# Optimization experiments

Measured on AMD Instinct MI355X. Metric: run time of the kernel, lower is better.

The kernel has to match this reference:

```python
import jax, jax.numpy as jnp
import numpy as np

LN_EPS = 1e-5


def _layernorm(h, gamma, beta):
    mu = jnp.mean(h, axis=-1, keepdims=True)
    var = jnp.var(h, axis=-1, keepdims=True)
    return (h - mu) * jax.lax.rsqrt(var + LN_EPS) * gamma + beta


def _simple_attention(q, k, v):
    # DIFFormer 'simple' kernel, num_heads=1: global-Frobenius-normalized q,k,
    # linear attention numerator + uniform component, denominator + N.
    n = q.shape[0]
    qs = q / jnp.linalg.norm(q)            # [N, M]
    ks = k / jnp.linalg.norm(k)            # [N, M]
    kvs = jnp.einsum('lm,ld->md', ks, v)   # [M, D]
    num = jnp.einsum('nm,md->nd', qs, kvs) + jnp.sum(v, axis=0)  # [N, D]
    den = jnp.einsum('nm,m->n', qs, jnp.sum(ks, axis=0)) + jnp.asarray(n, q.dtype)
    return num / den[:, None]


def reference(x, edge_index, W1, b1, Wq, bq, Wk, bk, gamma, beta, alpha, Wr, br, wgt):
    n = x.shape[0]
    row, col = edge_index[0], edge_index[1]
    # symmetric GCN normalization (degree of destination index, as in DIFFormer)
    deg = jax.ops.segment_sum(jnp.ones_like(col, dtype=x.dtype), col, num_segments=n)
    inv_sqrt = jnp.where(deg > 0, 1.0 / jnp.sqrt(deg), 0.0)
    w_edge = inv_sqrt[col] * inv_sqrt[row]  # [E]

    def gcn_conv(v):
        # out[i] = sum_{e: col[e]==i} w[e] * v[row[e]]
        return jax.ops.segment_sum(w_edge[:, None] * v[row], col, num_segments=n)

    def conv(h):
        q = h @ Wq + bq
        k = h @ Wk + bk
        v = h                              # use_weight=False -> value = source input
        return _simple_attention(q, k, v) + gcn_conv(v)

    R = jax.nn.relu(x @ W1 + b1)           # [N, H]
    Ts = [R]
    for _ in range(3):                      # three calls of the SAME shared conv
        Rn = conv(R)
        R = alpha * Rn + (1.0 - alpha) * R  # residual blend
        R = _layernorm(R, gamma, beta)      # shared LayerNorm
        Ts.append(R)

    # multi-head linear readout + learned weighted sum (dropout = identity in eval)
    res = jnp.stack([Ts[i] @ Wr[i] + br[i] for i in range(4)], axis=0)  # [4, N]
    out = jnp.einsum('i,in->n', wgt, res)[:, None]                       # [N, 1]
    return out


def setup_inputs():
    key = jax.random.key(0)
    ks = jax.random.split(key, 8)
    N, E, F_IN, H = 100000, 3200000, 58, 256
    x = jax.random.normal(ks[0], (N, F_IN), dtype=jnp.float32)
    edge_index = jax.random.randint(ks[1], (2, E), 0, N, dtype=jnp.int32)
    s_in = 1.0 / np.sqrt(F_IN)
    s_h = 1.0 / np.sqrt(H)
    return {
        'x': x,
        'edge_index': edge_index,
        'W1': jax.random.normal(ks[2], (F_IN, H), dtype=jnp.float32) * s_in,
        'b1': jnp.zeros((H,), jnp.float32),
        'Wq': jax.random.normal(ks[3], (H, H), dtype=jnp.float32) * s_h,
        'bq': jnp.zeros((H,), jnp.float32),
        'Wk': jax.random.normal(ks[4], (H, H), dtype=jnp.float32) * s_h,
        'bk': jnp.zeros((H,), jnp.float32),
        'gamma': jnp.ones((H,), jnp.float32),
        'beta': jnp.zeros((H,), jnp.float32),
        'alpha': jnp.float32(0.5),
        'Wr': jax.random.normal(ks[5], (4, H), dtype=jnp.float32) * s_h,
        'br': jnp.zeros((4,), jnp.float32),
        'wgt': jnp.array([0.5, 0.5, 0.5, 0.5], jnp.float32),
    }
```

## Files before the change

kernel.cpp:

```cpp
#include <hip/hip_runtime.h>

#define H 256
#define FIN 58
#define LN_EPS 1e-5f
#define ROWS_PB 384
#define EPB 8192
#define SBW 11

typedef __bf16 bf16x8 __attribute__((ext_vector_type(8)));
typedef float f32x16 __attribute__((ext_vector_type(16)));
typedef float f32x2 __attribute__((ext_vector_type(2)));

union FragU {
  ushort u[8];
  bf16x8 v;
};


__device__ __forceinline__ float wave_sum(float v) {
#pragma unroll
  for (int off = 1; off < 64; off <<= 1) v += __shfl_xor(v, off, 64);
  return v;
}

__device__ __forceinline__ float half_sum(float v) {
#pragma unroll
  for (int off = 1; off < 32; off <<= 1) v += __shfl_xor(v, off, 64);
  return v;
}

__device__ __forceinline__ float block_sum(float v, volatile float* red) {
  const int tid = threadIdx.x;
  v = wave_sum(v);
  __syncthreads();
  if ((tid & 63) == 0) red[tid >> 6] = v;
  __syncthreads();
  return red[0] + red[1] + red[2] + red[3];
}

__device__ __forceinline__ ushort f2bf(float f) {
  unsigned u = __float_as_uint(f);
  unsigned r = (u + 0x7FFFu + ((u >> 16) & 1u)) >> 16;
  return (ushort)r;
}

__device__ __forceinline__ float bf2f(ushort u) {
  return __uint_as_float((unsigned)u << 16);
}

#if __has_builtin(__builtin_amdgcn_cvt_pk_fp8_f32) && __has_builtin(__builtin_amdgcn_cvt_pk_f32_fp8)
__device__ __forceinline__ unsigned pack_fp8x4(float a, float b, float c, float d) {
  int v = 0;
  v = __builtin_amdgcn_cvt_pk_fp8_f32(a, b, v, false);
  v = __builtin_amdgcn_cvt_pk_fp8_f32(c, d, v, true);
  return (unsigned)v;
}
__device__ __forceinline__ void unpack_fp8x2_acc(f32x2& lo, f32x2& hi, unsigned v) {
  lo += __builtin_amdgcn_cvt_pk_f32_fp8((int)v, false);
  hi += __builtin_amdgcn_cvt_pk_f32_fp8((int)v, true);
}
#else
__device__ __forceinline__ unsigned char f2e4m3_1(float f) {
  unsigned u = __float_as_uint(f);
  unsigned s = (u >> 31) << 7;
  float a = fabsf(f);
  if (a >= 448.0f) return (unsigned char)(s | 0x7E);
  if (a < 0.0009765625f) return (unsigned char)s;
  int e;
  float m = frexpf(a, &e);
  int E = e - 1 + 7;
  if (E >= 1) {
    int mm = (int)rintf((m * 2.0f - 1.0f) * 8.0f);
    if (mm == 8) { mm = 0; E++; }
    return (unsigned char)(s | (E << 3) | mm);
  }
  int mm = (int)rintf(a * 512.0f);
  if (mm > 7) return (unsigned char)(s | (1 << 3));
  return (unsigned char)(s | mm);
}
__device__ __forceinline__ unsigned pack_fp8x4(float a, float b, float c, float d) {
  return (unsigned)f2e4m3_1(a) | ((unsigned)f2e4m3_1(b) << 8) |
         ((unsigned)f2e4m3_1(c) << 16) | ((unsigned)f2e4m3_1(d) << 24);
}
__device__ __forceinline__ float e4m3f_1(unsigned v) {
  int s = (v >> 7) & 1, E = (v >> 3) & 15, m = v & 7;
  float mag = E ? ldexpf(1.0f + m * 0.125f, E - 7) : ldexpf((float)m, -9);
  return s ? -mag : mag;
}
__device__ __forceinline__ void unpack_fp8x2_acc(f32x2& lo, f32x2& hi, unsigned v) {
  lo[0] += e4m3f_1(v & 255);
  lo[1] += e4m3f_1((v >> 8) & 255);
  hi[0] += e4m3f_1((v >> 16) & 255);
  hi[1] += e4m3f_1(v >> 24);
}
#endif


__global__ __launch_bounds__(512) void k_b1(const int* __restrict__ row,
                                            const int* __restrict__ col,
                                            unsigned* __restrict__ breg,
                                            int* __restrict__ gcnt,
                                            int cap2, int E, int nsb) {
  __shared__ unsigned stage[EPB];
  __shared__ int lh[65], lbase[65], lcur[64], gclaim[64];
  const int tid = threadIdx.x;
  const int e0 = blockIdx.x * EPB;
  const int cnt = min(EPB, E - e0);
  if (tid < 64) lh[tid] = 0;
  __syncthreads();
  for (int i = tid; i < cnt; i += 512) atomicAdd(&lh[col[e0 + i] >> SBW], 1);
  __syncthreads();
  if (tid == 0) {
    int acc = 0;
    for (int b = 0; b < nsb; b++) { lbase[b] = acc; acc += lh[b]; }
    lbase[nsb] = acc;
  }
  __syncthreads();
  if (tid < nsb) {
    gclaim[tid] = atomicAdd(&gcnt[tid], lh[tid]);
    lcur[tid] = lbase[tid];
  }
  __syncthreads();
  for (int i = tid; i < cnt; i += 512) {
    int c = col[e0 + i];
    int b = c >> SBW;
    int s = atomicAdd(&lcur[b], 1);
    stage[s] = ((unsigned)row[e0 + i] << SBW) | (unsigned)(c & ((1 << SBW) - 1));
  }
  __syncthreads();
  for (int i = tid; i < cnt; i += 512) {
    int lo = 0, hi = nsb;
    while (hi - lo > 1) {
      int mid = (lo + hi) >> 1;
      if (lbase[mid] <= i) lo = mid; else hi = mid;
    }
    int off = gclaim[lo] + (i - lbase[lo]);
    if (off < cap2) breg[(size_t)lo * cap2 + off] = stage[i];
  }
}

__global__ __launch_bounds__(512) void k_degB2(const unsigned* __restrict__ breg,
                                               const int* __restrict__ gcnt, int cap2,
                                               int* __restrict__ deg, int N) {
  __shared__ int lcnt[1 << SBW];
  const int b = blockIdx.x, tid = threadIdx.x, base = b << SBW;
  for (int i = tid; i < (1 << SBW); i += 512) lcnt[i] = 0;
  __syncthreads();
  const int cnt = min(gcnt[b], cap2);
  const unsigned* p = breg + (size_t)b * cap2;
  for (int i = tid; i < cnt; i += 512) atomicAdd(&lcnt[p[i] & ((1 << SBW) - 1)], 1);
  __syncthreads();
  for (int i = tid; i < (1 << SBW); i += 512) {
    int d = base + i;
    if (d < N) deg[d] = lcnt[i];
  }
}

__global__ __launch_bounds__(512) void k_b2(const unsigned* __restrict__ breg,
                                            const int* __restrict__ gcnt, int cap2,
                                            const int* __restrict__ offs16,
                                            int* __restrict__ eb, int N) {
  __shared__ int loffs[1 << SBW];
  __shared__ int lcur[1 << SBW];
  const int b = blockIdx.x, tid = threadIdx.x, base = b << SBW;
  for (int i = tid; i < (1 << SBW); i += 512) {
    int d = base + i;
    loffs[i] = (d < N) ? offs16[d] : 0;
    lcur[i] = 0;
  }
  __syncthreads();
  const int cnt = min(gcnt[b], cap2);
  const unsigned* p = breg + (size_t)b * cap2;
  for (int i = tid; i < cnt; i += 512) {
    unsigned rc = p[i];
    int lc = rc & ((1 << SBW) - 1);
    int slot = atomicAdd(&lcur[lc], 1);
    eb[loffs[lc] + slot] = (int)(rc >> SBW);
  }
  __syncthreads();
  for (int i = tid; i < (1 << SBW); i += 512) {
    int d = base + i;
    if (d < N) {
      int c = lcur[i];
      int pad = (c + 15) & ~15;
      int o = loffs[i];
      for (int j = c; j < pad; j++) eb[o + j] = N;
    }
  }
}

__global__ void k_invsqrt(const int* __restrict__ deg, float* __restrict__ invs, int N) {
  int i = blockIdx.x * 256 + threadIdx.x;
  if (i < N) {
    int d = deg[i];
    invs[i] = (d > 0) ? (1.0f / sqrtf((float)d)) : 0.0f;
  }
}

__global__ __launch_bounds__(1024) void k_scan1(const int* __restrict__ deg,
                                                int* __restrict__ offs16,
                                                int* __restrict__ bsum, int N) {
  __shared__ int buf[1024];
  const int tid = threadIdx.x;
  const int gid = blockIdx.x * 1024 + tid;
  int v = (gid < N) ? ((deg[gid] + 15) & ~15) : 0;
  buf[tid] = v;
  __syncthreads();
  for (int off = 1; off < 1024; off <<= 1) {
    int x = (tid >= off) ? buf[tid - off] : 0;
    __syncthreads();
    buf[tid] += x;
    __syncthreads();
  }
  if (gid < N) offs16[gid] = buf[tid] - v;
  if (tid == 1023) bsum[blockIdx.x] = buf[1023];
}

__global__ __launch_bounds__(1024) void k_scan2(int* __restrict__ bsum, int nb) {
  __shared__ int buf[1024];
  const int tid = threadIdx.x;
  int v = (tid < nb) ? bsum[tid] : 0;
  buf[tid] = v;
  __syncthreads();
  for (int off = 1; off < 1024; off <<= 1) {
    int x = (tid >= off) ? buf[tid - off] : 0;
    __syncthreads();
    buf[tid] += x;
    __syncthreads();
  }
  if (tid < nb) bsum[tid] = buf[tid] - v;
}

__global__ void k_scan3(int* __restrict__ offs16, const int* __restrict__ bsum, int N) {
  int i = blockIdx.x * 256 + threadIdx.x;
  if (i < N) offs16[i] += bsum[i >> 10];
}

__global__ void k_prep(const float* __restrict__ Wq, const float* __restrict__ Wk,
                       const float* __restrict__ bq, const float* __restrict__ bk,
                       float* __restrict__ P, float* __restrict__ Q, float* __restrict__ K2,
                       float* __restrict__ pb, float* __restrict__ qb,
                       float* __restrict__ wb, float* __restrict__ kb,
                       float* __restrict__ sconst) {
  __shared__ float red[4];
  const int b = blockIdx.x, tid = threadIdx.x;
  if (b < 768) {
    const int f = b & 255, which = b >> 8;
    const float* A = (which == 2) ? Wk : Wq;
    const float* Bm = (which == 1) ? Wq : Wk;
    float acc = 0.0f;
    for (int m = 0; m < H; m++) acc = fmaf(A[f * H + m], Bm[tid * H + m], acc);
    float* D = (which == 0) ? P : ((which == 1) ? Q : K2);
    D[f * H + tid] = acc;
  } else {
    float a1 = 0, a2 = 0, a3 = 0, a4 = 0;
    for (int m = 0; m < H; m++) {
      float wqv = Wq[tid * H + m], wkv = Wk[tid * H + m];
      a1 = fmaf(wqv, bk[m], a1);
      a2 = fmaf(wqv, bq[m], a2);
      a3 = fmaf(wkv, bq[m], a3);
      a4 = fmaf(wkv, bk[m], a4);
    }
    pb[tid] = a1; qb[tid] = a2; wb[tid] = a3; kb[tid] = a4;
    float c0 = block_sum(bq[tid] * bk[tid], red);
    float c1 = block_sum(bq[tid] * bq[tid], red);
    float c2 = block_sum(bk[tid] * bk[tid], red);
    if (tid == 0) { sconst[0] = c0; sconst[1] = c1; sconst[2] = c2; }
  }
}

__global__ void k_fc1(const float* __restrict__ x, const float* __restrict__ W1,
                      const float* __restrict__ b1, const float* __restrict__ Wr,
                      const float* __restrict__ br, const float* __restrict__ wgt,
                      ushort* __restrict__ R0, float* __restrict__ out, int N) {
  __shared__ __align__(16) float lx[16 * FIN];
  __shared__ float red2[4][16];
  const int tid = threadIdx.x;
  const int n0 = blockIdx.x * 16;
  for (int idx = tid; idx < 16 * FIN / 4; idx += 256)
    ((float4*)lx)[idx] = ((const float4*)(x + (size_t)n0 * FIN))[idx];
  __syncthreads();
  float acc[16];
  const float bias = b1[tid];
#pragma unroll
  for (int r = 0; r < 16; r++) acc[r] = bias;
  for (int f = 0; f < FIN; f++) {
    float wv = W1[f * H + tid];
#pragma unroll
    for (int r = 0; r < 16; r++) acc[r] = fmaf(lx[r * FIN + f], wv, acc[r]);
  }
  const float wr0 = Wr[tid];
#pragma unroll
  for (int r = 0; r < 16; r++) {
    acc[r] = fmaxf(acc[r], 0.0f);
    int n = n0 + r;
    if (n < N) R0[(size_t)n * H + tid] = f2bf(acc[r]);
  }
#pragma unroll
  for (int r = 0; r < 16; r++) {
    float s = wave_sum(acc[r] * wr0);
    if ((tid & 63) == 0) red2[tid >> 6][r] = s;
  }
  __syncthreads();
  if (tid < 16) {
    int n = n0 + tid;
    if (n < N)
      out[n] = wgt[0] * (red2[0][tid] + red2[1][tid] + red2[2][tid] + red2[3][tid] + br[0]);
  }
}

__global__ __launch_bounds__(512, 2) void k_Gm(const ushort* __restrict__ Rb,
                                               const float* __restrict__ invs,
                                               ushort* __restrict__ Gslab,
                                               unsigned* __restrict__ Rf8,
                                               float* __restrict__ vsum, int N) {
  __shared__ ushort sb[2][32 * 256];
  const int tid = threadIdx.x;
  const int lane = tid & 63;
  const int wid = tid >> 6;
  const int wrow = (wid & 1) * 128;
  const int wcol = (wid >> 1) * 64;
  const int l31 = lane & 31;
  const int lhi = lane >> 5;

  const int rowbase = blockIdx.x * ROWS_PB;
  const int nrows = min(ROWS_PB, N - rowbase);
  const int nch = (nrows + 31) >> 5;

  const int sk = tid >> 4;
  const int c0 = (tid & 15) * 16;

  f32x16 acc[4][2];
#pragma unroll
  for (int s = 0; s < 4; s++)
#pragma unroll
    for (int t = 0; t < 2; t++)
#pragma unroll
      for (int e = 0; e < 16; e++) acc[s][t][e] = 0.0f;

  float csum[16];
#pragma unroll
  for (int i = 0; i < 16; i++) csum[i] = 0.0f;

  int4 ld[2];

  auto load_chunk = [&](int ch) {
    int g = rowbase + ch * 32 + sk;
    const int4* src = (const int4*)(Rb + (size_t)g * H + c0);
    ld[0] = (g < N) ? src[0] : make_int4(0, 0, 0, 0);
    ld[1] = (g < N) ? src[1] : make_int4(0, 0, 0, 0);
  };

  auto write_chunk = [&](int ch, int buf) {
    int g = rowbase + ch * 32 + sk;
    const int swz = (sk & 3) << 4;
    const float sc = (g < N) ? invs[g] : 0.0f;
    unsigned w8[4];
#pragma unroll
    for (int i = 0; i < 2; i++) {
      *(int4*)&sb[buf][sk * 256 + ((c0 + 8 * i) ^ swz)] = ld[i];
      const ushort* pu = (const ushort*)&ld[i];
#pragma unroll
      for (int j = 0; j < 8; j++) csum[8 * i + j] += bf2f(pu[j]);
      w8[2 * i] = pack_fp8x4(bf2f(pu[0]) * sc, bf2f(pu[1]) * sc,
                             bf2f(pu[2]) * sc, bf2f(pu[3]) * sc);
      w8[2 * i + 1] = pack_fp8x4(bf2f(pu[4]) * sc, bf2f(pu[5]) * sc,
                                 bf2f(pu[6]) * sc, bf2f(pu[7]) * sc);
    }
    if (g < N)
      *(uint4*)&Rf8[(size_t)g * 64 + (c0 >> 2)] = make_uint4(w8[0], w8[1], w8[2], w8[3]);
  };

  auto compute = [&](int buf) {
#pragma unroll
    for (int ks = 0; ks < 2; ks++) {
      const int kb = ks * 16 + lhi * 8;
      FragU fr[6];
#pragma unroll
      for (int s = 0; s < 6; s++) {
        const int cbase = (s < 4) ? (wrow + 32 * s + l31) : (wcol + 32 * (s - 4) + l31);
#pragma unroll
        for (int j = 0; j < 8; j++)
          fr[s].u[j] = sb[buf][(kb + j) * 256 + (cbase ^ ((j & 3) << 4))];
      }
#pragma unroll
      for (int s = 0; s < 4; s++)
#pragma unroll
        for (int t = 0; t < 2; t++)
          acc[s][t] = __builtin_amdgcn_mfma_f32_32x32x16_bf16(fr[s].v, fr[4 + t].v,
                                                              acc[s][t], 0, 0, 0);
    }
  };

  if (nch > 0) {
    load_chunk(0);
    write_chunk(0, 0);
    __syncthreads();
    int cur = 0;
    for (int c = 0; c < nch; c++) {
      if (c + 1 < nch) load_chunk(c + 1);
      compute(cur);
      if (c + 1 < nch) write_chunk(c + 1, cur ^ 1);
      __syncthreads();
      cur ^= 1;
    }
  }

  ushort* Gs = Gslab + (size_t)blockIdx.x * 65536;
#pragma unroll
  for (int s = 0; s < 4; s++)
#pragma unroll
    for (int t = 0; t < 2; t++) {
      const int n0c = wcol + 32 * t + l31;
#pragma unroll
      for (int r = 0; r < 16; r++) {
        const int row = wrow + 32 * s + (r & 3) + 8 * (r >> 2) + 4 * lhi;
        Gs[row * 256 + n0c] = f2bf(acc[s][t][r]);
      }
    }

  float* fl = (float*)sb;
#pragma unroll
  for (int j = 0; j < 16; j++) fl[sk * 256 + c0 + j] = csum[j];
  __syncthreads();
  if (tid < 256) {
    float s = 0.0f;
    for (int r = 0; r < 32; r++) s += fl[r * 256 + tid];
    atomicAdd(&vsum[tid], s);
  }
}

__global__ void k_Gr(const ushort* __restrict__ Gslab, float* __restrict__ G, int nslab) {
  const int i = blockIdx.x * 256 + threadIdx.x;
  float s0 = 0, s1 = 0, s2 = 0, s3 = 0;
  int b = 0;
  for (; b + 3 < nslab; b += 4) {
    s0 += bf2f(Gslab[(size_t)b * 65536 + i]);
    s1 += bf2f(Gslab[(size_t)(b + 1) * 65536 + i]);
    s2 += bf2f(Gslab[(size_t)(b + 2) * 65536 + i]);
    s3 += bf2f(Gslab[(size_t)(b + 3) * 65536 + i]);
  }
  float s = s0 + s1 + s2 + s3;
  for (; b < nslab; b++) s += bf2f(Gslab[(size_t)b * 65536 + i]);
  G[i] = s;
}

__global__ void k_small(const float* __restrict__ G, const float* __restrict__ vsum,
                        const float* __restrict__ P, const float* __restrict__ pb,
                        const float* __restrict__ wb, const float* __restrict__ sconst,
                        const float* __restrict__ Q, const float* __restrict__ K2,
                        ushort* __restrict__ Mt, float* __restrict__ cvec,
                        float* __restrict__ dvec, float* __restrict__ scal, int N) {
  __shared__ float red[4];
  const int b = blockIdx.x, tid = threadIdx.x;
  if (b < 256) {
    float acc = 0.0f;
    for (int m = 0; m < H; m++) acc = fmaf(P[b * H + m], G[m * H + tid], acc);
    Mt[(size_t)tid * H + b] = f2bf(acc + pb[b] * vsum[tid]);
  } else if (b == 256) {
    float acc = 0.0f;
    for (int f = 0; f < H; f++) acc = fmaf(wb[f], G[f * H + tid], acc);
    cvec[tid] = acc + sconst[0] * vsum[tid];
  } else if (b == 257) {
    float acc = 0.0f;
    for (int m = 0; m < H; m++) acc = fmaf(P[tid * H + m], vsum[m], acc);
    dvec[tid] = acc + (float)N * pb[tid];
  } else if (b < 274) {
    int base = (b - 258) * 4096 + tid;
    float a = 0.0f;
    for (int j = 0; j < 16; j++) a = fmaf(G[base + j * 256], Q[base + j * 256], a);
    a = block_sum(a, red);
    if (tid == 0) atomicAdd(&scal[0], a);
  } else {
    int base = (b - 274) * 4096 + tid;
    float a = 0.0f;
    for (int j = 0; j < 16; j++) a = fmaf(G[base + j * 256], K2[base + j * 256], a);
    a = block_sum(a, red);
    if (tid == 0) atomicAdd(&scal[1], a);
  }
}

__global__ void k_final(const float* __restrict__ vsum, const float* __restrict__ qb,
                        const float* __restrict__ kb, const float* __restrict__ wb,
                        const float* __restrict__ sconst, float* __restrict__ scal, int N) {
  __shared__ float red[4];
  const int tid = threadIdx.x;
  float s1 = block_sum(qb[tid] * vsum[tid], red);
  float s2 = block_sum(kb[tid] * vsum[tid], red);
  float s3 = block_sum(wb[tid] * vsum[tid], red);
  if (tid == 0) {
    float sq = scal[0] + 2.0f * s1 + (float)N * sconst[1];
    float sk = scal[1] + 2.0f * s2 + (float)N * sconst[2];
    scal[2] = 1.0f / (sqrtf(sq) * sqrtf(sk));
    scal[3] = s3 + (float)N * sconst[0];
  }
}

__global__ __launch_bounds__(512) void k_N(const ushort* __restrict__ Rb,
                                           const ushort* __restrict__ Mt,
                                           ushort* __restrict__ numb, int N) {
  const int tid = threadIdx.x;
  const int lane = tid & 63;
  const int wid = tid >> 6;
  const int l31 = lane & 31;
  const int lhi = lane >> 5;
  const int wrow = (wid & 3) * 32;
  const int wcol = (wid >> 2) * 128;
  const int rowbase = blockIdx.x * 128;

  f32x16 acc[4];
#pragma unroll
  for (int t = 0; t < 4; t++)
#pragma unroll
    for (int e = 0; e < 16; e++) acc[t][e] = 0.0f;

  const ushort* aptr = Rb + (size_t)(rowbase + wrow + l31) * H;

  for (int kc = 0; kc < 16; kc++) {
    const int kb = kc * 16 + lhi * 8;
    FragU fa;
    *(int4*)fa.u = *(const int4*)(aptr + kb);
    FragU fb0, fb1, fb2, fb3;
    *(int4*)fb0.u = *(const int4*)(Mt + (size_t)(wcol + 0 + l31) * H + kb);
    *(int4*)fb1.u = *(const int4*)(Mt + (size_t)(wcol + 32 + l31) * H + kb);
    *(int4*)fb2.u = *(const int4*)(Mt + (size_t)(wcol + 64 + l31) * H + kb);
    *(int4*)fb3.u = *(const int4*)(Mt + (size_t)(wcol + 96 + l31) * H + kb);
    acc[0] = __builtin_amdgcn_mfma_f32_32x32x16_bf16(fa.v, fb0.v, acc[0], 0, 0, 0);
    acc[1] = __builtin_amdgcn_mfma_f32_32x32x16_bf16(fa.v, fb1.v, acc[1], 0, 0, 0);
    acc[2] = __builtin_amdgcn_mfma_f32_32x32x16_bf16(fa.v, fb2.v, acc[2], 0, 0, 0);
    acc[3] = __builtin_amdgcn_mfma_f32_32x32x16_bf16(fa.v, fb3.v, acc[3], 0, 0, 0);
  }

#pragma unroll
  for (int t = 0; t < 4; t++) {
    const int col = wcol + 32 * t + l31;
#pragma unroll
    for (int r = 0; r < 16; r++) {
      const int row = rowbase + wrow + (r & 3) + 8 * (r >> 2) + 4 * lhi;
      if (row < N) numb[(size_t)row * H + col] = f2bf(acc[t][r]);
    }
  }
}

__global__ __launch_bounds__(256) void k_C(
    const ushort* __restrict__ Rb, ushort* __restrict__ Rnext,
    const ushort* __restrict__ numb, const unsigned* __restrict__ Rf8,
    const int* __restrict__ eb, const float* __restrict__ invs,
    const float* __restrict__ cvec, const float* __restrict__ dvec,
    const float* __restrict__ vsum, const float* __restrict__ scal,
    const int* __restrict__ offs16, const int* __restrict__ deg,
    const float* __restrict__ alphap, const float* __restrict__ gamma,
    const float* __restrict__ beta, const float* __restrict__ Wr,
    const float* __restrict__ br, const float* __restrict__ wgt,
    float* __restrict__ out, int N, int layer, int last) {
  const int tid = threadIdx.x, lane = tid & 63, wv = tid >> 6;
  const int half = lane >> 5, hl = lane & 31;
  const int d0 = hl * 8;
  const int n0 = blockIdx.x * 32 + wv * 8;

  const float invn = scal[2], denc = scal[3];
  const float al = alphap[0], om = 1.0f - al;
  const float4 dvA = *(const float4*)&dvec[d0];
  const float4 dvB = *(const float4*)&dvec[d0 + 4];
  const float4 cvA = *(const float4*)&cvec[d0];
  const float4 cvB = *(const float4*)&cvec[d0 + 4];
  const float4 vsA = *(const float4*)&vsum[d0];
  const float4 vsB = *(const float4*)&vsum[d0 + 4];
  const float4 gmA = *(const float4*)&gamma[d0];
  const float4 gmB = *(const float4*)&gamma[d0 + 4];
  const float4 btA = *(const float4*)&beta[d0];
  const float4 btB = *(const float4*)&beta[d0 + 4];
  const float4 wrA = *(const float4*)&Wr[layer * H + d0];
  const float4 wrB = *(const float4*)&Wr[layer * H + d0 + 4];
  const float wl = wgt[layer], bl = br[layer];

  for (int r = 0; r < 4; r++) {
    const int n = n0 + r * 2 + half;
    const bool valid = n < N;
    const int ns = valid ? n : 0;

    const int4 rv = *(const int4*)&Rb[(size_t)ns * H + d0];
    const int4 nv = *(const int4*)&numb[(size_t)ns * H + d0];
    const ushort* rp = (const ushort*)&rv;
    const ushort* np = (const ushort*)&nv;
    float old[8], num[8];
#pragma unroll
    for (int j = 0; j < 8; j++) { old[j] = bf2f(rp[j]); num[j] = bf2f(np[j]); }

    float p = old[0] * dvA.x + old[1] * dvA.y + old[2] * dvA.z + old[3] * dvA.w +
              old[4] * dvB.x + old[5] * dvB.y + old[6] * dvB.z + old[7] * dvB.w;
    p = half_sum(p);
    const float rden = 1.0f / ((p + denc) * invn + (float)N);

    f32x2 a01 = {0.f, 0.f}, a23 = {0.f, 0.f}, a45 = {0.f, 0.f}, a67 = {0.f, 0.f};
    const int st = offs16[ns];
    const int nbch = valid ? ((deg[ns] + 15) >> 4) : 0;
    const int4* pe = (const int4*)(eb + st);
    const int woff = hl * 2;
    for (int b = 0; b < nbch; b++, pe += 4) {
      int4 q0 = pe[0], q1 = pe[1], q2 = pe[2], q3 = pe[3];
      const int srcs[16] = {q0.x, q0.y, q0.z, q0.w, q1.x, q1.y, q1.z, q1.w,
                            q2.x, q2.y, q2.z, q2.w, q3.x, q3.y, q3.z, q3.w};
      uint2 g[16];
#pragma unroll
      for (int i = 0; i < 16; i++)
        g[i] = *(const uint2*)&Rf8[((size_t)srcs[i] << 6) + woff];
#pragma unroll
      for (int i = 0; i < 16; i++) {
        unpack_fp8x2_acc(a01, a23, g[i].x);
        unpack_fp8x2_acc(a45, a67, g[i].y);
      }
    }
    const float sn = invs[ns];
    float ag[8] = {a01[0] * sn, a01[1] * sn, a23[0] * sn, a23[1] * sn,
                   a45[0] * sn, a45[1] * sn, a67[0] * sn, a67[1] * sn};

    const float cva[8] = {cvA.x, cvA.y, cvA.z, cvA.w, cvB.x, cvB.y, cvB.z, cvB.w};
    const float vsa[8] = {vsA.x, vsA.y, vsA.z, vsA.w, vsB.x, vsB.y, vsB.z, vsB.w};
    float hv[8];
#pragma unroll
    for (int j = 0; j < 8; j++)
      hv[j] = al * (((num[j] + cva[j]) * invn + vsa[j]) * rden + ag[j]) + om * old[j];

    float s = 0.0f, s2 = 0.0f;
#pragma unroll
    for (int j = 0; j < 8; j++) { s += hv[j]; s2 += hv[j] * hv[j]; }
    s = half_sum(s);
    s2 = half_sum(s2);
    const float mu = s * (1.0f / H);
    const float var = s2 * (1.0f / H) - mu * mu;
    const float rs = rsqrtf(var + LN_EPS);

    const float gma[8] = {gmA.x, gmA.y, gmA.z, gmA.w, gmB.x, gmB.y, gmB.z, gmB.w};
    const float bta[8] = {btA.x, btA.y, btA.z, btA.w, btB.x, btB.y, btB.z, btB.w};
    const float wra[8] = {wrA.x, wrA.y, wrA.z, wrA.w, wrB.x, wrB.y, wrB.z, wrB.w};
    float y[8], rp2 = 0.0f;
    ushort yo[8];
#pragma unroll
    for (int j = 0; j < 8; j++) {
      y[j] = (hv[j] - mu) * rs * gma[j] + bta[j];
      yo[j] = f2bf(y[j]);
      rp2 += y[j] * wra[j];
    }
    if (!last && valid) *(int4*)&Rnext[(size_t)n * H + d0] = *(int4*)yo;
    rp2 = half_sum(rp2);
    if (hl == 0 && valid) out[n] += wl * (rp2 + bl);
  }
}


extern "C" void kernel_launch(void* const* d_in, const int* in_sizes, int n_in,
                              void* d_out, int out_size, void* d_ws, size_t ws_size,
                              hipStream_t stream) {
  const float* x = (const float*)d_in[0];
  const int* ei = (const int*)d_in[1];
  const float* W1 = (const float*)d_in[2];
  const float* b1 = (const float*)d_in[3];
  const float* Wq = (const float*)d_in[4];
  const float* bq = (const float*)d_in[5];
  const float* Wk = (const float*)d_in[6];
  const float* bk = (const float*)d_in[7];
  const float* gamma = (const float*)d_in[8];
  const float* beta = (const float*)d_in[9];
  const float* alphap = (const float*)d_in[10];
  const float* Wr = (const float*)d_in[11];
  const float* br = (const float*)d_in[12];
  const float* wgt = (const float*)d_in[13];
  float* out = (float*)d_out;

  const int N = in_sizes[0] / FIN;
  const int E = in_sizes[1] / 2;
  const int* row = ei;
  const int* col = ei + E;

  char* w = (char*)d_ws;
  auto alloc = [&](size_t bytes) -> char* {
    char* p = w;
    w += (bytes + 255) & ~(size_t)255;
    return p;
  };
  const size_t RB = (size_t)(N + 128) * H * sizeof(ushort);
  ushort* Rb0 = (ushort*)alloc(RB);
  ushort* Rb1 = (ushort*)alloc(RB);
  ushort* numb = (ushort*)alloc(RB);
  unsigned* Rf8 = (unsigned*)alloc((size_t)(N + 1) * 64 * sizeof(unsigned));
  ushort* Mt = (ushort*)alloc(H * H * sizeof(ushort));
  float* G = (float*)alloc(H * H * sizeof(float));
  float* vsum = (float*)alloc(1024);
  float* scal = (float*)alloc(256);
  float* cvec = (float*)alloc(1024);
  float* dvec = (float*)alloc(1024);
  float* P = (float*)alloc(H * H * sizeof(float));
  float* Q = (float*)alloc(H * H * sizeof(float));
  float* K2 = (float*)alloc(H * H * sizeof(float));
  float* pb = (float*)alloc(1024);
  float* qb = (float*)alloc(1024);
  float* wb = (float*)alloc(1024);
  float* kb = (float*)alloc(1024);
  float* sconst = (float*)alloc(256);
  int* deg = (int*)alloc((size_t)N * 4);
  float* invs = (float*)alloc((size_t)N * 4);
  int* offs16 = (int*)alloc((size_t)(N + 1) * 4);
  int* bsum = (int*)alloc(1024 * 4);
  int* gcnt = (int*)alloc(64 * 4);
  size_t EPAD = (size_t)E + 16 * (size_t)N;
  EPAD = (EPAD + 3) & ~(size_t)3;
  int* eb = (int*)alloc(EPAD * sizeof(int));

  const int NSB = (N + (1 << SBW) - 1) >> SBW;
  int cap2 = (E / (NSB > 0 ? NSB : 1)) * 2 + 4096;
  cap2 = (cap2 + 3) & ~3;
  unsigned* breg = (unsigned*)Rb1;
  ushort* Gslab = (ushort*)numb;

  hipMemsetAsync(gcnt, 0, 64 * 4, stream);
  hipMemsetAsync(Rf8 + (size_t)N * 64, 0, 64 * sizeof(unsigned), stream);

  const int gN = (N + 255) / 256;
  const int nblk = (N + 1023) / 1024;
  const int nbB1 = (E + EPB - 1) / EPB;
  k_b1<<<nbB1, 512, 0, stream>>>(row, col, breg, gcnt, cap2, E, NSB);
  k_degB2<<<NSB, 512, 0, stream>>>(breg, gcnt, cap2, deg, N);
  k_invsqrt<<<gN, 256, 0, stream>>>(deg, invs, N);
  k_scan1<<<nblk, 1024, 0, stream>>>(deg, offs16, bsum, N);
  k_scan2<<<1, 1024, 0, stream>>>(bsum, nblk);
  k_scan3<<<gN, 256, 0, stream>>>(offs16, bsum, N);
  k_b2<<<NSB, 512, 0, stream>>>(breg, gcnt, cap2, offs16, eb, N);
  k_prep<<<769, 256, 0, stream>>>(Wq, Wk, bq, bk, P, Q, K2, pb, qb, wb, kb, sconst);
  const int gRows16 = (N + 15) / 16;
  k_fc1<<<gRows16, 256, 0, stream>>>(x, W1, b1, Wr, br, wgt, Rb0, out, N);

  const int nbG = (N + ROWS_PB - 1) / ROWS_PB;
  const int nbN = (N + 127) / 128;
  const int gRows32 = (N + 31) / 32;
  ushort* Rc = Rb0;
  ushort* Rn = Rb1;
  for (int it = 1; it <= 3; ++it) {
    hipMemsetAsync(vsum, 0, 1024 + 256, stream);
    k_Gm<<<nbG, 512, 0, stream>>>(Rc, invs, Gslab, Rf8, vsum, N);
    k_Gr<<<256, 256, 0, stream>>>(Gslab, G, nbG);
    k_small<<<290, 256, 0, stream>>>(G, vsum, P, pb, wb, sconst, Q, K2, Mt, cvec, dvec, scal, N);
    k_final<<<1, 256, 0, stream>>>(vsum, qb, kb, wb, sconst, scal, N);
    k_N<<<nbN, 512, 0, stream>>>(Rc, Mt, numb, N);
    k_C<<<gRows32, 256, 0, stream>>>(Rc, Rn, numb, Rf8, eb, invs, cvec, dvec, vsum, scal,
                                     offs16, deg, alphap, gamma, beta, Wr, br, wgt, out,
                                     N, it, (it == 3) ? 1 : 0);
    ushort* t = Rc; Rc = Rn; Rn = t;
  }
}
```

Before: 1.212 ms.

## Fuse small preprocessing kernels and transpose Gram staging layout in LDS

Folds the inverse-sqrt-degree computation into the degree kernel and the scan offset fix-up into the bucket-fill kernel, which removes two launches. The per-iteration memset, the atomics, the Frobenius dot-product blocks and k_final are replaced by per-block column-sum slabs that k_Gr reduces, with k_small finishing the scalars, so each iteration issues fewer launches. k_Gm now stages rows transposed (feature-major) in shared memory so each MFMA fragment loads with one 16-byte read instead of eight scalar reads. The risks are new LDS bank-conflict patterns on the transposed writes and more serial reduction work per block in k_Gr.

```diff
diff --git a/kernel.cpp b/kernel.cpp
--- a/kernel.cpp
+++ b/kernel.cpp
@@ -141,7 +141,8 @@
 
 __global__ __launch_bounds__(512) void k_degB2(const unsigned* __restrict__ breg,
                                                const int* __restrict__ gcnt, int cap2,
-                                               int* __restrict__ deg, int N) {
+                                               int* __restrict__ deg,
+                                               float* __restrict__ invs, int N) {
   __shared__ int lcnt[1 << SBW];
   const int b = blockIdx.x, tid = threadIdx.x, base = b << SBW;
   for (int i = tid; i < (1 << SBW); i += 512) lcnt[i] = 0;
@@ -152,20 +153,31 @@
   __syncthreads();
   for (int i = tid; i < (1 << SBW); i += 512) {
     int d = base + i;
-    if (d < N) deg[d] = lcnt[i];
+    if (d < N) {
+      int c = lcnt[i];
+      deg[d] = c;
+      invs[d] = (c > 0) ? (1.0f / sqrtf((float)c)) : 0.0f;
+    }
   }
 }
 
 __global__ __launch_bounds__(512) void k_b2(const unsigned* __restrict__ breg,
                                             const int* __restrict__ gcnt, int cap2,
-                                            const int* __restrict__ offs16,
+                                            int* __restrict__ offs16,
+                                            const int* __restrict__ bsum,
                                             int* __restrict__ eb, int N) {
   __shared__ int loffs[1 << SBW];
   __shared__ int lcur[1 << SBW];
   const int b = blockIdx.x, tid = threadIdx.x, base = b << SBW;
   for (int i = tid; i < (1 << SBW); i += 512) {
     int d = base + i;
-    loffs[i] = (d < N) ? offs16[d] : 0;
+    if (d < N) {
+      int o = offs16[d] + bsum[d >> 10];
+      loffs[i] = o;
+      offs16[d] = o;
+    } else {
+      loffs[i] = 0;
+    }
     lcur[i] = 0;
   }
   __syncthreads();
@@ -186,14 +198,6 @@
       int o = loffs[i];
       for (int j = c; j < pad; j++) eb[o + j] = N;
     }
-  }
-}
-
-__global__ void k_invsqrt(const int* __restrict__ deg, float* __restrict__ invs, int N) {
-  int i = blockIdx.x * 256 + threadIdx.x;
-  if (i < N) {
-    int d = deg[i];
-    invs[i] = (d > 0) ? (1.0f / sqrtf((float)d)) : 0.0f;
   }
 }
 
@@ -229,11 +233,6 @@
     __syncthreads();
   }
   if (tid < nb) bsum[tid] = buf[tid] - v;
-}
-
-__global__ void k_scan3(int* __restrict__ offs16, const int* __restrict__ bsum, int N) {
-  int i = blockIdx.x * 256 + threadIdx.x;
-  if (i < N) offs16[i] += bsum[i >> 10];
 }
 
 __global__ void k_prep(const float* __restrict__ Wq, const float* __restrict__ Wk,
@@ -313,8 +312,8 @@
                                                const float* __restrict__ invs,
                                                ushort* __restrict__ Gslab,
                                                unsigned* __restrict__ Rf8,
-                                               float* __restrict__ vsum, int N) {
-  __shared__ ushort sb[2][32 * 256];
+                                               float* __restrict__ csl, int N) {
+  __shared__ ushort sbT[2][256 * 32];
   const int tid = threadIdx.x;
   const int lane = tid & 63;
   const int wid = tid >> 6;
@@ -327,8 +326,9 @@
   const int nrows = min(ROWS_PB, N - rowbase);
   const int nch = (nrows + 31) >> 5;
 
-  const int sk = tid >> 4;
-  const int c0 = (tid & 15) * 16;
+  const int rp = tid >> 5;
+  const int fg = tid & 31;
+  const int k2 = rp * 2;
 
   f32x16 acc[4][2];
 #pragma unroll
@@ -338,50 +338,64 @@
 #pragma unroll
       for (int e = 0; e < 16; e++) acc[s][t][e] = 0.0f;
 
-  float csum[16];
-#pragma unroll
-  for (int i = 0; i < 16; i++) csum[i] = 0.0f;
-
-  int4 ld[2];
+  float cs[8];
+#pragma unroll
+  for (int i = 0; i < 8; i++) cs[i] = 0.0f;
+
+  int4 la, lb;
+  float sc0, sc1;
 
   auto load_chunk = [&](int ch) {
-    int g = rowbase + ch * 32 + sk;
-    const int4* src = (const int4*)(Rb + (size_t)g * H + c0);
-    ld[0] = (g < N) ? src[0] : make_int4(0, 0, 0, 0);
-    ld[1] = (g < N) ? src[1] : make_int4(0, 0, 0, 0);
+    int g0 = rowbase + ch * 32 + k2;
+    const int4* s0 = (const int4*)(Rb + (size_t)g0 * H + fg * 8);
+    const int4* s1 = (const int4*)(Rb + (size_t)(g0 + 1) * H + fg * 8);
+    la = (g0 < N) ? s0[0] : make_int4(0, 0, 0, 0);
+    lb = (g0 + 1 < N) ? s1[0] : make_int4(0, 0, 0, 0);
+    sc0 = (g0 < N) ? invs[g0] : 0.0f;
+    sc1 = (g0 + 1 < N) ? invs[g0 + 1] : 0.0f;
   };
 
   auto write_chunk = [&](int ch, int buf) {
-    int g = rowbase + ch * 32 + sk;
-    const int swz = (sk & 3) << 4;
-    const float sc = (g < N) ? invs[g] : 0.0f;
-    unsigned w8[4];
-#pragma unroll
-    for (int i = 0; i < 2; i++) {
-      *(int4*)&sb[buf][sk * 256 + ((c0 + 8 * i) ^ swz)] = ld[i];
-      const ushort* pu = (const ushort*)&ld[i];
-#pragma unroll
-      for (int j = 0; j < 8; j++) csum[8 * i + j] += bf2f(pu[j]);
-      w8[2 * i] = pack_fp8x4(bf2f(pu[0]) * sc, bf2f(pu[1]) * sc,
-                             bf2f(pu[2]) * sc, bf2f(pu[3]) * sc);
-      w8[2 * i + 1] = pack_fp8x4(bf2f(pu[4]) * sc, bf2f(pu[5]) * sc,
-                                 bf2f(pu[6]) * sc, bf2f(pu[7]) * sc);
-    }
-    if (g < N)
-      *(uint4*)&Rf8[(size_t)g * 64 + (c0 >> 2)] = make_uint4(w8[0], w8[1], w8[2], w8[3]);
+    int g0 = rowbase + ch * 32 + k2;
+    const ushort* pa = (const ushort*)&la;
+    const ushort* pbu = (const ushort*)&lb;
+    const int blk = (k2 & 24) ^ ((fg & 3) << 3);
+    uint* dst = (uint*)sbT[buf];
+#pragma unroll
+    for (int i = 0; i < 8; i++) {
+      float av = bf2f(pa[i]), bv = bf2f(pbu[i]);
+      cs[i] += av + bv;
+      unsigned val = (unsigned)pa[i] | ((unsigned)pbu[i] << 16);
+      int f = fg * 8 + i;
+      dst[f * 16 + ((blk + (k2 & 7)) >> 1)] = val;
+    }
+    if (g0 < N) {
+      unsigned w0 = pack_fp8x4(bf2f(pa[0]) * sc0, bf2f(pa[1]) * sc0,
+                               bf2f(pa[2]) * sc0, bf2f(pa[3]) * sc0);
+      unsigned w1 = pack_fp8x4(bf2f(pa[4]) * sc0, bf2f(pa[5]) * sc0,
+                               bf2f(pa[6]) * sc0, bf2f(pa[7]) * sc0);
+      *(uint2*)&Rf8[(size_t)g0 * 64 + fg * 2] = make_uint2(w0, w1);
+    }
+    if (g0 + 1 < N) {
+      unsigned w0 = pack_fp8x4(bf2f(pbu[0]) * sc1, bf2f(pbu[1]) * sc1,
+                               bf2f(pbu[2]) * sc1, bf2f(pbu[3]) * sc1);
+      unsigned w1 = pack_fp8x4(bf2f(pbu[4]) * sc1, bf2f(pbu[5]) * sc1,
+                               bf2f(pbu[6]) * sc1, bf2f(pbu[7]) * sc1);
+      *(uint2*)&Rf8[(size_t)(g0 + 1) * 64 + fg * 2] = make_uint2(w0, w1);
+    }
   };
 
   auto compute = [&](int buf) {
+    const ushort* bp = sbT[buf];
 #pragma unroll
     for (int ks = 0; ks < 2; ks++) {
       const int kb = ks * 16 + lhi * 8;
       FragU fr[6];
 #pragma unroll
       for (int s = 0; s < 6; s++) {
-        const int cbase = (s < 4) ? (wrow + 32 * s + l31) : (wcol + 32 * (s - 4) + l31);
-#pragma unroll
-        for (int j = 0; j < 8; j++)
-          fr[s].u[j] = sb[buf][(kb + j) * 256 + (cbase ^ ((j & 3) << 4))];
+        const int cb = (s < 4) ? (wrow + 32 * s + l31) : (wcol + 32 * (s - 4) + l31);
+        const int off = cb * 32 + (kb ^ (((cb >> 3) & 3) << 3));
+        *(int4*)fr[s].u = *(const int4*)(bp + off);
       }
 #pragma unroll
       for (int s = 0; s < 4; s++)
@@ -419,36 +433,50 @@
       }
     }
 
-  float* fl = (float*)sb;
-#pragma unroll
-  for (int j = 0; j < 16; j++) fl[sk * 256 + c0 + j] = csum[j];
+  __syncthreads();
+  float* fl = (float*)sbT;
+#pragma unroll
+  for (int i = 0; i < 8; i++) fl[rp * 256 + fg * 8 + i] = cs[i];
   __syncthreads();
   if (tid < 256) {
-    float s = 0.0f;
-    for (int r = 0; r < 32; r++) s += fl[r * 256 + tid];
-    atomicAdd(&vsum[tid], s);
-  }
-}
-
-__global__ void k_Gr(const ushort* __restrict__ Gslab, float* __restrict__ G, int nslab) {
-  const int i = blockIdx.x * 256 + threadIdx.x;
+    float v = 0.0f;
+    for (int j = 0; j < 16; j++) v += fl[j * 256 + tid];
+    csl[(size_t)blockIdx.x * 256 + tid] = v;
+  }
+}
+
+__global__ void k_Gr(const ushort* __restrict__ Gslab, const float* __restrict__ csl,
+                     const float* __restrict__ Q, const float* __restrict__ K2,
+                     float* __restrict__ G, float* __restrict__ vsum,
+                     float2* __restrict__ spart, int nslab) {
+  __shared__ float red[4];
+  const int b = blockIdx.x, t = threadIdx.x;
+  const int i = b * 256 + t;
   float s0 = 0, s1 = 0, s2 = 0, s3 = 0;
-  int b = 0;
-  for (; b + 3 < nslab; b += 4) {
-    s0 += bf2f(Gslab[(size_t)b * 65536 + i]);
-    s1 += bf2f(Gslab[(size_t)(b + 1) * 65536 + i]);
-    s2 += bf2f(Gslab[(size_t)(b + 2) * 65536 + i]);
-    s3 += bf2f(Gslab[(size_t)(b + 3) * 65536 + i]);
+  int j = 0;
+  for (; j + 3 < nslab; j += 4) {
+    s0 += bf2f(Gslab[(size_t)j * 65536 + i]);
+    s1 += bf2f(Gslab[(size_t)(j + 1) * 65536 + i]);
+    s2 += bf2f(Gslab[(size_t)(j + 2) * 65536 + i]);
+    s3 += bf2f(Gslab[(size_t)(j + 3) * 65536 + i]);
   }
   float s = s0 + s1 + s2 + s3;
-  for (; b < nslab; b++) s += bf2f(Gslab[(size_t)b * 65536 + i]);
+  for (; j < nslab; j++) s += bf2f(Gslab[(size_t)j * 65536 + i]);
   G[i] = s;
+  float dq = block_sum(s * Q[i], red);
+  float dk = block_sum(s * K2[i], red);
+  if (t == 0) spart[b] = make_float2(dq, dk);
+  float v = 0.0f;
+  for (int u = t; u < nslab; u += 256) v += csl[(size_t)u * 256 + b];
+  v = block_sum(v, red);
+  if (t == 0) vsum[b] = v;
 }
 
 __global__ void k_small(const float* __restrict__ G, const float* __restrict__ vsum,
                         const float* __restrict__ P, const float* __restrict__ pb,
                         const float* __restrict__ wb, const float* __restrict__ sconst,
-                        const float* __restrict__ Q, const float* __restrict__ K2,
+                        const float* __restrict__ qb, const float* __restrict__ kbv,
+                        const float2* __restrict__ spart,
                         ushort* __restrict__ Mt, float* __restrict__ cvec,
                         float* __restrict__ dvec, float* __restrict__ scal, int N) {
   __shared__ float red[4];
@@ -465,34 +493,19 @@
     float acc = 0.0f;
     for (int m = 0; m < H; m++) acc = fmaf(P[tid * H + m], vsum[m], acc);
     dvec[tid] = acc + (float)N * pb[tid];
-  } else if (b < 274) {
-    int base = (b - 258) * 4096 + tid;
-    float a = 0.0f;
-    for (int j = 0; j < 16; j++) a = fmaf(G[base + j * 256], Q[base + j * 256], a);
-    a = block_sum(a, red);
-    if (tid == 0) atomicAdd(&scal[0], a);
   } else {
-    int base = (b - 274) * 4096 + tid;
-    float a = 0.0f;
-    for (int j = 0; j < 16; j++) a = fmaf(G[base + j * 256], K2[base + j * 256], a);
-    a = block_sum(a, red);
-    if (tid == 0) atomicAdd(&scal[1], a);
-  }
-}
-
-__global__ void k_final(const float* __restrict__ vsum, const float* __restrict__ qb,
-                        const float* __restrict__ kb, const float* __restrict__ wb,
-                        const float* __restrict__ sconst, float* __restrict__ scal, int N) {
-  __shared__ float red[4];
-  const int tid = threadIdx.x;
-  float s1 = block_sum(qb[tid] * vsum[tid], red);
-  float s2 = block_sum(kb[tid] * vsum[tid], red);
-  float s3 = block_sum(wb[tid] * vsum[tid], red);
-  if (tid == 0) {
-    float sq = scal[0] + 2.0f * s1 + (float)N * sconst[1];
-    float sk = scal[1] + 2.0f * s2 + (float)N * sconst[2];
-    scal[2] = 1.0f / (sqrtf(sq) * sqrtf(sk));
-    scal[3] = s3 + (float)N * sconst[0];
+    float2 sp = spart[tid];
+    float dq = block_sum(sp.x, red);
+    float dk = block_sum(sp.y, red);
+    float s1 = block_sum(qb[tid] * vsum[tid], red);
+    float s2 = block_sum(kbv[tid] * vsum[tid], red);
+    float s3 = block_sum(wb[tid] * vsum[tid], red);
+    if (tid == 0) {
+      float sq = dq + 2.0f * s1 + (float)N * sconst[1];
+      float sk = dk + 2.0f * s2 + (float)N * sconst[2];
+      scal[2] = 1.0f / (sqrtf(sq) * sqrtf(sk));
+      scal[3] = s3 + (float)N * sconst[0];
+    }
   }
 }
 
@@ -703,6 +716,9 @@
   int* offs16 = (int*)alloc((size_t)(N + 1) * 4);
   int* bsum = (int*)alloc(1024 * 4);
   int* gcnt = (int*)alloc(64 * 4);
+  const int nbG = (N + ROWS_PB - 1) / ROWS_PB;
+  float* csl = (float*)alloc((size_t)nbG * 256 * sizeof(float));
+  float2* spart = (float2*)alloc(256 * sizeof(float2));
   size_t EPAD = (size_t)E + 16 * (size_t)N;
   EPAD = (EPAD + 3) & ~(size_t)3;
   int* eb = (int*)alloc(EPAD * sizeof(int));
@@ -716,31 +732,26 @@
   hipMemsetAsync(gcnt, 0, 64 * 4, stream);
   hipMemsetAsync(Rf8 + (size_t)N * 64, 0, 64 * sizeof(unsigned), stream);
 
-  const int gN = (N + 255) / 256;
   const int nblk = (N + 1023) / 1024;
   const int nbB1 = (E + EPB - 1) / EPB;
   k_b1<<<nbB1, 512, 0, stream>>>(row, col, breg, gcnt, cap2, E, NSB);
-  k_degB2<<<NSB, 512, 0, stream>>>(breg, gcnt, cap2, deg, N);
-  k_invsqrt<<<gN, 256, 0, stream>>>(deg, invs, N);
+  k_degB2<<<NSB, 512, 0, stream>>>(breg, gcnt, cap2, deg, invs, N);
   k_scan1<<<nblk, 1024, 0, stream>>>(deg, offs16, bsum, N);
   k_scan2<<<1, 1024, 0, stream>>>(bsum, nblk);
-  k_scan3<<<gN, 256, 0, stream>>>(offs16, bsum, N);
-  k_b2<<<NSB, 512, 0, stream>>>(breg, gcnt, cap2, offs16, eb, N);
+  k_b2<<<NSB, 512, 0, stream>>>(breg, gcnt, cap2, offs16, bsum, eb, N);
   k_prep<<<769, 256, 0, stream>>>(Wq, Wk, bq, bk, P, Q, K2, pb, qb, wb, kb, sconst);
   const int gRows16 = (N + 15) / 16;
   k_fc1<<<gRows16, 256, 0, stream>>>(x, W1, b1, Wr, br, wgt, Rb0, out, N);
 
-  const int nbG = (N + ROWS_PB - 1) / ROWS_PB;
   const int nbN = (N + 127) / 128;
   const int gRows32 = (N + 31) / 32;
   ushort* Rc = Rb0;
   ushort* Rn = Rb1;
   for (int it = 1; it <= 3; ++it) {
-    hipMemsetAsync(vsum, 0, 1024 + 256, stream);
-    k_Gm<<<nbG, 512, 0, stream>>>(Rc, invs, Gslab, Rf8, vsum, N);
-    k_Gr<<<256, 256, 0, stream>>>(Gslab, G, nbG);
-    k_small<<<290, 256, 0, stream>>>(G, vsum, P, pb, wb, sconst, Q, K2, Mt, cvec, dvec, scal, N);
-    k_final<<<1, 256, 0, stream>>>(vsum, qb, kb, wb, sconst, scal, N);
+    k_Gm<<<nbG, 512, 0, stream>>>(Rc, invs, Gslab, Rf8, csl, N);
+    k_Gr<<<256, 256, 0, stream>>>(Gslab, csl, Q, K2, G, vsum, spart, nbG);
+    k_small<<<259, 256, 0, stream>>>(G, vsum, P, pb, wb, sconst, qb, kb, spart,
+                                     Mt, cvec, dvec, scal, N);
     k_N<<<nbN, 512, 0, stream>>>(Rc, Mt, numb, N);
     k_C<<<gRows32, 256, 0, stream>>>(Rc, Rn, numb, Rf8, eb, invs, cvec, dvec, vsum, scal,
                                      offs16, deg, alphap, gamma, beta, Wr, br, wgt, out,
```

Measured after the change: 1.163 ms. 4.1% less time.
